# Optimization experiments

Measured on AMD Instinct MI355X. Metric: run time of the kernel, lower is better.

The kernel has to match this reference:

```python
import jax, jax.numpy as jnp
import numpy as np

N = 768          # nodes
E_HALF = 12288   # undirected edges (both directions added -> E = 24576)
P = 4096         # query pairs
H = 32           # hidden_dim_1wl == hidden_dim_2wl
MAX_X = 100
EPS = 1e-5
LAYER1 = 2


def setup_inputs() -> dict:
    key = jax.random.key(0)
    ks = jax.random.split(key, 12)
    s = 0.1
    x = jax.random.randint(ks[0], (N,), 0, MAX_X + 1)
    half = jax.random.randint(ks[1], (2, E_HALF), 0, N)
    ei = jnp.concatenate([half, half[::-1]], axis=1)          # symmetric edge set [2,E]
    pos = jax.random.randint(ks[2], (P, 2), 0, N)
    emb = jax.random.normal(ks[3], (MAX_X + 1, H)) * s
    gcn_W = jax.random.normal(ks[4], (LAYER1, H, H)) * s
    gcn_b = jnp.zeros((LAYER1, H))
    mlp1_W = jax.random.normal(ks[5], (2 * H, H)) * s
    mlp1_b = jnp.zeros((H,))
    mlp2_W = jax.random.normal(ks[6], (2 * H, H)) * s
    mlp2_b = jnp.zeros((H,))
    mlp3_W = jax.random.normal(ks[7], (H + 1, H)) * s
    mlp3_b = jnp.zeros((H,))
    lin_W = jax.random.normal(ks[8], (2 * H, 1)) * s
    lin_b = jnp.zeros((1,))
    return dict(x=x, ei=ei, pos=pos, emb=emb, gcn_W=gcn_W, gcn_b=gcn_b,
                mlp1_W=mlp1_W, mlp1_b=mlp1_b, mlp2_W=mlp2_W, mlp2_b=mlp2_b,
                mlp3_W=mlp3_W, mlp3_b=mlp3_b, lin_W=lin_W, lin_b=lin_b)


def _graph_norm(h):
    # PyG-style GraphNorm with default params (mean_scale=1, weight=1, bias=0)
    h = h - h.mean(0)
    return h * jax.lax.rsqrt((h * h).mean(0) + EPS)


def reference(x, ei, pos, emb, gcn_W, gcn_b, mlp1_W, mlp1_b,
              mlp2_W, mlp2_b, mlp3_W, mlp3_b, lin_W, lin_b):
    n = x.shape[0]
    d = emb.shape[1]
    h = emb[x]                                                 # [n,H] (dropout=0)
    # --- GCNConv stack: Ahat = D^-1/2 (A+I) D^-1/2 ---
    A = jnp.zeros((n, n), h.dtype).at[ei[0], ei[1]].set(1.0)
    Ahat = A + jnp.eye(n, dtype=h.dtype)
    dinv = jax.lax.rsqrt(Ahat.sum(1))
    An = Ahat * dinv[:, None] * dinv[None, :]
    for l in range(gcn_W.shape[0]):
        h = An @ (h @ gcn_W[l]) + gcn_b[l]
        h = jax.nn.relu(_graph_norm(h))                        # GraphNorm + ReLU
    # --- pair features ---
    xx = h[pos[:, 0]] * h[pos[:, 1]]                           # [P,H]
    val = jnp.concatenate([h[ei[0]], h[ei[1]]], 1)             # [E,2H]
    xe = jax.nn.relu(val @ mlp1_W + mlp1_b)                    # mlps_1
    mul = jax.nn.relu(val @ mlp2_W + mlp2_b)                   # mlps_2[0]
    # --- sparse_bmm as dense [n,n,d] contraction (coalesce sums duplicates -> .add) ---
    Xd = jnp.zeros((n, n, d), h.dtype).at[ei[0], ei[1]].add(xe)
    Md = jnp.zeros((n, n, d), h.dtype).at[ei[0], ei[1]].add(mul)
    C = jnp.einsum('ikd,kjd->ijd', Xd, Md)                     # x_{ij} = sum_k x_{ik}*mul_{kj}
    # support of the sparse result: 2-hop pairs union original edges (sparse_cat)
    adj_b = jnp.zeros((n, n), bool).at[ei[0], ei[1]].set(True)
    af = adj_b.astype(h.dtype)
    mask = ((af @ af) > 0) | adj_b
    ind = af[..., None]                                        # ones-column for original edges
    value = jnp.concatenate([C, ind], -1)                      # [n,n,H+1]
    z = value @ mlp3_W + mlp3_b                                # mlps_3[0]
    # GraphNorm over the edge support only (faithful to sparse values())
    m = mask.astype(h.dtype)[..., None]
    cnt = m.sum()
    mean = (z * m).sum((0, 1)) / cnt
    z = z - mean
    var = ((z * z) * m).sum((0, 1)) / cnt
    z = jax.nn.relu(z * jax.lax.rsqrt(var + EPS))
    # x * sm: multiply by transposed values; zero outside support (= add_zero)
    sym = z * jnp.swapaxes(z, 0, 1) * m
    pair = sym[pos[:, 0], pos[:, 1]]                           # [P,H] (edge_list gather)
    out = jnp.concatenate([pair, xx], 1) @ lin_W + lin_b       # lin_dir -> [P,1]
    return out
```

## Files before the change

kernel.cpp:

```cpp
#include <hip/hip_runtime.h>
#include <hip/hip_bf16.h>

#define NN 768
#define NE 24576
#define NPOS 4096
#define NCELL (NN*NN)
#define NBLK 2304
#define NBIG 2304
#define BCELLS 256
#define CAP 4
#define NREP 16

typedef __hip_bfloat16 bf16;

__device__ __forceinline__ float ldf(const void* p, int i, int mode) {
    return mode ? __bfloat162float(((const bf16*)p)[i]) : ((const float*)p)[i];
}
__device__ __forceinline__ float aread(float* p) { return atomicAdd(p, 0.f); }
__device__ __forceinline__ int areadi(int* p) { return atomicAdd(p, 0); }

template<int D, int HALF>
__device__ __forceinline__ void redRound(float* v, int lane) {
#pragma unroll
    for (int i = 0; i < HALF; i++) {
        float snd = (lane & D) ? v[i] : v[i + HALF];
        float r = __shfl_xor(snd, D);
        v[i] = ((lane & D) ? v[i + HALF] : v[i]) + r;
    }
}

#define DOT4(Z, A, W) Z += A.x * W.x + A.y * W.y + A.z * W.z + A.w * W.w

#define BLO(u) __uint_as_float((u) << 16)
#define BHI(u) __uint_as_float((u) & 0xFFFF0000u)

#define GATHB(rec, q0,q1,q2,q3,q4,q5,q6,q7) { \
    const uint4* xr = xep4b + (int)((unsigned)(rec).x & 0x7FFFu) * 4; \
    const uint4* mr = mulp4b + (int)((unsigned)(rec).y & 0x7FFFu) * 4; \
    uint4 xA = xr[0], xB = xr[1], xC = xr[2], xD = xr[3]; \
    uint4 mA = mr[0], mB = mr[1], mC = mr[2], mD = mr[3]; \
    q0.x += BLO(xA.x)*BLO(mA.x); q0.y += BHI(xA.x)*BHI(mA.x); \
    q0.z += BLO(xA.y)*BLO(mA.y); q0.w += BHI(xA.y)*BHI(mA.y); \
    q1.x += BLO(xA.z)*BLO(mA.z); q1.y += BHI(xA.z)*BHI(mA.z); \
    q1.z += BLO(xA.w)*BLO(mA.w); q1.w += BHI(xA.w)*BHI(mA.w); \
    q2.x += BLO(xB.x)*BLO(mB.x); q2.y += BHI(xB.x)*BHI(mB.x); \
    q2.z += BLO(xB.y)*BLO(mB.y); q2.w += BHI(xB.y)*BHI(mB.y); \
    q3.x += BLO(xB.z)*BLO(mB.z); q3.y += BHI(xB.z)*BHI(mB.z); \
    q3.z += BLO(xB.w)*BLO(mB.w); q3.w += BHI(xB.w)*BHI(mB.w); \
    q4.x += BLO(xC.x)*BLO(mC.x); q4.y += BHI(xC.x)*BHI(mC.x); \
    q4.z += BLO(xC.y)*BLO(mC.y); q4.w += BHI(xC.y)*BHI(mC.y); \
    q5.x += BLO(xC.z)*BLO(mC.z); q5.y += BHI(xC.z)*BHI(mC.z); \
    q5.z += BLO(xC.w)*BLO(mC.w); q5.w += BHI(xC.w)*BHI(mC.w); \
    q6.x += BLO(xD.x)*BLO(mD.x); q6.y += BHI(xD.x)*BHI(mD.x); \
    q6.z += BLO(xD.y)*BLO(mD.y); q6.w += BHI(xD.y)*BHI(mD.y); \
    q7.x += BLO(xD.z)*BLO(mD.z); q7.y += BHI(xD.z)*BHI(mD.z); \
    q7.z += BLO(xD.w)*BLO(mD.w); q7.w += BHI(xD.w)*BHI(mD.w); }

__global__ void k_scatter(const int* __restrict__ ei, int* __restrict__ cell, int* __restrict__ rowlen,
                          int* __restrict__ row_ptr, float* __restrict__ dinv, int* __restrict__ dc,
                          const void* __restrict__ gW, const void* __restrict__ gB,
                          const void* __restrict__ m1W, const void* __restrict__ m1B,
                          const void* __restrict__ m2W, const void* __restrict__ m2B,
                          const void* __restrict__ m3W, const void* __restrict__ m3B,
                          const void* __restrict__ lW,  const void* __restrict__ lB,
                          const void* __restrict__ emb, int* __restrict__ modeg,
                          float* __restrict__ gwf, float* __restrict__ gbf,
                          float* __restrict__ w1f, float* __restrict__ b1f,
                          float* __restrict__ w2f, float* __restrict__ b2f,
                          float* __restrict__ w3q, float* __restrict__ linf, float* __restrict__ linb) {
    int t = threadIdx.x;
    if (blockIdx.x == 96) {
        __shared__ int bad;
        if (t == 0) bad = 0;
        __syncthreads();
        int local = 0;
        for (int i = t; i < 3232; i += 256) {
            float a = fabsf(__bfloat162float(((const bf16*)emb)[i]));
            if (!(a < 100.f)) local = 1;
        }
        if (local) atomicOr(&bad, 1);
        __syncthreads();
        int mode = bad ? 0 : 1;
        if (t == 0) *modeg = mode;
        for (int i = t; i < 2048; i += 256) {
            gwf[i] = ldf(gW, i, mode);
            w1f[i] = ldf(m1W, i, mode);
            w2f[i] = ldf(m2W, i, mode);
        }
        for (int i = t; i < 64; i += 256) { gbf[i] = ldf(gB, i, mode); linf[i] = ldf(lW, i, mode); }
        if (t < 32) { b1f[t] = ldf(m1B, t, mode); b2f[t] = ldf(m2B, t, mode); }
        for (int i = t; i < 1056; i += 256) { int c = i >> 5, d = i & 31; w3q[d * 36 + c] = ldf(m3W, i, mode); }
        if (t < 32) { w3q[t * 36 + 33] = ldf(m3B, t, mode); w3q[t * 36 + 34] = 0.f; w3q[t * 36 + 35] = 0.f; }
        if (t == 0) linb[0] = ldf(lB, 0, mode);
        return;
    }
    __shared__ int amlast;
    __shared__ int sI[256];
    int e = blockIdx.x * 256 + t;
    int a = ei[e], b = ei[NE + e];
    if ((unsigned)a < (unsigned)NN && (unsigned)b < (unsigned)NN) {
        int old = atomicAdd(&cell[a * NN + b], 1);
        if (old == 0) atomicAdd(&rowlen[a], 1);
    }
    __syncthreads();
    if (t == 0) { __threadfence(); amlast = (atomicAdd(dc, 1) == 95) ? 1 : 0; }
    __syncthreads();
    if (!amlast) return;
    int i0 = 3 * t;
    int r0 = areadi(&rowlen[i0]), r1 = areadi(&rowlen[i0 + 1]), r2 = areadi(&rowlen[i0 + 2]);
    dinv[i0]     = rsqrtf((float)r0 + 1.f);
    dinv[i0 + 1] = rsqrtf((float)r1 + 1.f);
    dinv[i0 + 2] = rsqrtf((float)r2 + 1.f);
    int s3 = r0 + r1 + r2;
    sI[t] = s3;
    __syncthreads();
    for (int off = 1; off < 256; off <<= 1) {
        int tmp = (t >= off) ? sI[t - off] : 0;
        __syncthreads();
        sI[t] += tmp;
        __syncthreads();
    }
    int excl = sI[t] - s3;
    row_ptr[i0] = excl;
    row_ptr[i0 + 1] = excl + r0;
    row_ptr[i0 + 2] = excl + r0 + r1;
    if (t == 255) row_ptr[NN] = sI[255];
}

__global__ void k_fill(int* __restrict__ cell, const int* __restrict__ row_ptr, int* __restrict__ cursor,
                       int* __restrict__ col_idx, float* __restrict__ cntv, int* __restrict__ pr_row,
                       const int* __restrict__ rowlen, int* __restrict__ rtot,
                       const int* __restrict__ x, const void* __restrict__ emb,
                       const int* __restrict__ modep, float* __restrict__ bufA) {
    int t = threadIdx.x;
    int b = blockIdx.x;
    if (b < NBLK) {
        int idx = b * 256 + t;
        int i = idx / NN;
        int j = idx - i * NN;
        int cv = cell[idx];
        if (cv > 0) {
            int p = row_ptr[i] + atomicAdd(&cursor[i], 1);
            col_idx[p] = j; cntv[p] = (float)cv; pr_row[p] = i;
            cell[idx] = p;
            atomicAdd(&rtot[i], rowlen[j]);
        } else cell[idx] = -1;
    } else {
        int idx = (b - NBLK) * 256 + t;
        int i = idx >> 5, k = idx & 31;
        int xi = x[i]; if (xi < 0) xi = 0; if (xi > 100) xi = 100;
        bufA[idx] = ldf(emb, xi * 32 + k, *modep);
    }
}

__global__ void k_aggmw0(const int* __restrict__ rtot, int* __restrict__ row_base,
                         const int* __restrict__ row_ptr, const int* __restrict__ col_idx,
                         const float* __restrict__ bufA, const float* __restrict__ dinv,
                         const float* __restrict__ gwf, const float* __restrict__ gbf,
                         float* __restrict__ bufB) {
    int t = threadIdx.x;
    if (blockIdx.x == 0) {
        __shared__ int sI[256];
        int r3[3]; int s3 = 0;
#pragma unroll
        for (int q = 0; q < 3; q++) { r3[q] = rtot[3 * t + q]; s3 += r3[q]; }
        sI[t] = s3;
        __syncthreads();
        for (int off = 1; off < 256; off <<= 1) {
            int tmp = (t >= off) ? sI[t - off] : 0;
            __syncthreads();
            sI[t] += tmp;
            __syncthreads();
        }
        int run = sI[t] - s3;
        row_base[3 * t] = run;
        row_base[3 * t + 1] = run + r3[0];
        row_base[3 * t + 2] = run + r3[0] + r3[1];
        return;
    }
    __shared__ float sg8[8][32];
    __shared__ float agg[32];
    int sgi = t >> 5, k = t & 31;
    int i = blockIdx.x - 1;
    int base = row_ptr[i], len = row_ptr[i + 1] - base;
    float di = dinv[i];
    float acc = (sgi == 0) ? di * bufA[i * 32 + k] : 0.f;
    for (int e = sgi; e < len; e += 8) {
        int c = col_idx[base + e];
        acc += dinv[c] * bufA[c * 32 + k];
    }
    sg8[sgi][k] = acc;
    __syncthreads();
    if (t < 32) {
        float s = 0.f;
#pragma unroll
        for (int q = 0; q < 8; q++) s += sg8[q][k];
        agg[k] = di * s;
    }
    __syncthreads();
    if (t < 32) {
        int d = k;
        float s = gbf[d];
#pragma unroll
        for (int kk = 0; kk < 32; kk++) s += agg[kk] * gwf[kk * 32 + d];
        bufB[i * 32 + d] = s;
    }
}

__global__ void k_hist(const int* __restrict__ row_ptr, const int* __restrict__ col_idx,
                       const int* __restrict__ row_base,
                       int* __restrict__ pcur, int2* __restrict__ paths2, int cap,
                       const float* __restrict__ bufB, const float* __restrict__ dinv,
                       const float* __restrict__ gwf, const float* __restrict__ gbf,
                       float* __restrict__ bufA, float* __restrict__ stats1) {
    __shared__ float r1[256], r2[256];
    __shared__ float nmean[32], nrstd[32];
    __shared__ int hist[NN];
    __shared__ int sc[256];
    __shared__ float sg8[8][32];
    __shared__ float agg[32];
    int t = threadIdx.x;
    int i = blockIdx.x;

    {
        int dd = t & 31, g = t >> 5;
        float s = 0.f, s2 = 0.f;
        for (int r = g; r < NN; r += 8) { float v = bufB[r * 32 + dd]; s += v; s2 += v * v; }
        r1[t] = s; r2[t] = s2;
        __syncthreads();
        if (t < 32) {
            float a = 0.f, b2 = 0.f;
            for (int k = 0; k < 8; k++) { a += r1[k * 32 + t]; b2 += r2[k * 32 + t]; }
            float mean = a / (float)NN;
            float var = b2 / (float)NN - mean * mean;
            nmean[t] = mean;
            nrstd[t] = rsqrtf(fmaxf(var, 0.f) + 1e-5f);
        }
    }

    int base = row_ptr[i], len = row_ptr[i + 1] - base;
    int rb = row_base[i];
    int wave = t >> 6, lane = t & 63;
    int sub = lane >> 5, l2 = lane & 31;
    for (int j = t; j < NN; j += 256) hist[j] = 0;
    __syncthreads();

    for (int ee = wave * 2 + sub; ee < len; ee += 8) {
        int k = col_idx[base + ee];
        int kb = row_ptr[k], ke = row_ptr[k + 1];
        for (int e = kb + l2; e < ke; e += 32) atomicAdd(&hist[col_idx[e]], 1);
    }
    __syncthreads();
    int h0 = hist[3 * t], h1 = hist[3 * t + 1], h2 = hist[3 * t + 2];
    int s3 = h0 + h1 + h2;
    sc[t] = s3;
    __syncthreads();
    for (int off = 1; off < 256; off <<= 1) {
        int tmp = (t >= off) ? sc[t - off] : 0;
        __syncthreads();
        sc[t] += tmp;
        __syncthreads();
    }
    int excl = sc[t] - s3;
    int n0 = i * NN + 3 * t;
    pcur[n0]     = rb + excl + h0;
    pcur[n0 + 1] = rb + excl + h0 + h1;
    pcur[n0 + 2] = rb + excl + h0 + h1 + h2;
    hist[3 * t] = excl;
    hist[3 * t + 1] = excl + h0;
    hist[3 * t + 2] = excl + h0 + h1;
    __syncthreads();

    for (int ee = wave * 2 + sub; ee < len; ee += 8) {
        int e1 = base + ee;
        int k = col_idx[e1];
        int kb = row_ptr[k], ke = row_ptr[k + 1];
        for (int e = kb + l2; e < ke; e += 32) {
            int j = col_idx[e];
            int slot = rb + atomicAdd(&hist[j], 1);
            if (slot < cap) {
                unsigned n2 = (unsigned)(i * NN + j);
                paths2[slot] = make_int2((int)((unsigned)e1 | ((n2 & 0x1FFFFu) << 15)),
                                         (int)((unsigned)e  | ((n2 >> 17) << 15)));
            }
        }
    }
    __syncthreads();

    {
        int sgi = t >> 5, k = t & 31;
        float mk = nmean[k], rk = nrstd[k];
        float di = dinv[i];
        float acc = (sgi == 0) ? di * fmaxf((bufB[i * 32 + k] - mk) * rk, 0.f) : 0.f;
        for (int e = sgi; e < len; e += 8) {
            int c = col_idx[base + e];
            acc += dinv[c] * fmaxf((bufB[c * 32 + k] - mk) * rk, 0.f);
        }
        sg8[sgi][k] = acc;
        __syncthreads();
        if (t < 32) {
            float s = 0.f;
#pragma unroll
            for (int q = 0; q < 8; q++) s += sg8[q][k];
            agg[k] = di * s;
        }
        __syncthreads();
        if (t < 32) {
            int d = k;
            const float* W = gwf + 1024;
            float s = gbf[32 + d];
#pragma unroll
            for (int kk = 0; kk < 32; kk++) s += agg[kk] * W[kk * 32 + d];
            bufA[i * 32 + d] = s;
            float* rep = stats1 + (blockIdx.x & (NREP - 1)) * 80;
            atomicAdd(&rep[d], s);
            atomicAdd(&rep[32 + d], s * s);
        }
    }
}

__global__ void k_emlp(const float* __restrict__ bufA, const float* __restrict__ stats1,
                       const int* __restrict__ row_ptr, const int* __restrict__ col_idx,
                       const int* __restrict__ pr_row, const float* __restrict__ cntv,
                       const float* __restrict__ w1f, const float* __restrict__ b1f,
                       const float* __restrict__ w2f, const float* __restrict__ b2f,
                       bf16* __restrict__ xepb, bf16* __restrict__ mulpb, float* __restrict__ h) {
    __shared__ float nmean[32], nrstd[32];
    int t = threadIdx.x;
    int b = blockIdx.x;
    if (t < 32) {
        float s = 0.f, s2 = 0.f;
#pragma unroll
        for (int r = 0; r < NREP; r++) { s += stats1[r * 80 + t]; s2 += stats1[r * 80 + 32 + t]; }
        float mean = s / (float)NN;
        float var = s2 / (float)NN - mean * mean;
        nmean[t] = mean;
        nrstd[t] = rsqrtf(fmaxf(var, 0.f) + 1e-5f);
    }
    __syncthreads();
    if (b < 3072) {
        int d = t & 31;
        int p = b * 8 + (t >> 5);
        if (p >= row_ptr[NN]) {
            if (p < NE) { xepb[p * 32 + d] = __float2bfloat16(0.f); mulpb[p * 32 + d] = __float2bfloat16(0.f); }
            return;
        }
        int i = pr_row[p], j = col_idx[p];
        float a1 = b1f[d], a2 = b2f[d];
#pragma unroll
        for (int c = 0; c < 32; c++) {
            float hv = fmaxf((bufA[i * 32 + c] - nmean[c]) * nrstd[c], 0.f);
            a1 += hv * w1f[c * 32 + d];
            a2 += hv * w2f[c * 32 + d];
        }
#pragma unroll
        for (int c = 0; c < 32; c++) {
            float hv = fmaxf((bufA[j * 32 + c] - nmean[c]) * nrstd[c], 0.f);
            a1 += hv * w1f[(32 + c) * 32 + d];
            a2 += hv * w2f[(32 + c) * 32 + d];
        }
        float cv = cntv[p];
        xepb[p * 32 + d]  = __float2bfloat16(cv * fmaxf(a1, 0.f));
        mulpb[p * 32 + d] = __float2bfloat16(cv * fmaxf(a2, 0.f));
    } else {
        int idx = (b - 3072) * 256 + t;
        int d = idx & 31;
        h[idx] = fmaxf((bufA[idx] - nmean[d]) * nrstd[d], 0.f);
    }
}

__global__ __launch_bounds__(256, 4) void k_big(const int* __restrict__ pcur,
                                                const int2* __restrict__ paths2,
                                                const int* __restrict__ cellA,
                                                const bf16* __restrict__ xepb, const bf16* __restrict__ mulpb,
                                                const float* __restrict__ w3q,
                                                float* __restrict__ stats, int* __restrict__ done,
                                                float* __restrict__ nrm, int cap) {
    __shared__ float qbuf[64 * 32];
    __shared__ int qps[64], qpe[64];
    __shared__ float sS1[32], sS2[32];
    __shared__ float sCm;
    __shared__ int amlast;
    __shared__ int qcnt;
    const uint4* xep4b = (const uint4*)xepb;
    const uint4* mulp4b = (const uint4*)mulpb;
    int t = threadIdx.x;
    int b = blockIdx.x;
    int cell0 = b * BCELLS;
    int wid = t >> 6, lane = t & 63, half = lane >> 5, d = lane & 31;

    if (t == 0) { sCm = 0.f; qcnt = 0; }
    if (t < 32) { sS1[t] = 0.f; sS2[t] = 0.f; }
    int myn = cell0 + t;
    int mp1 = pcur[myn];
    int mp0 = (myn == 0) ? 0 : pcur[myn - 1];
    int madj = cellA[myn];
    if (mp0 > cap) mp0 = cap;
    if (mp1 > cap) mp1 = cap;
    __syncthreads();

    int len = mp1 - mp0;
    int take = (len > CAP) ? CAP : len;
    int myq = -1;
    if (len > CAP) {
        int s = atomicAdd(&qcnt, 1);
        if (s < 64) { myq = s; qps[s] = mp0 + CAP; qpe[s] = mp1; }
    }
    int pm = cap - 1; if (pm < 0) pm = 0;
    int i0 = mp0, i1 = mp0 + 1, i2 = mp0 + 2, i3 = mp0 + 3;
    if (i0 > pm) i0 = pm; if (i1 > pm) i1 = pm; if (i2 > pm) i2 = pm; if (i3 > pm) i3 = pm;
    int2 r0 = paths2[i0];
    int2 r1 = paths2[i1];
    int2 r2 = paths2[i2];
    int2 r3 = paths2[i3];
    float4 q0 = {0.f,0.f,0.f,0.f}, q1 = q0, q2 = q0, q3 = q0, q4 = q0, q5 = q0, q6 = q0, q7 = q0;
    if (take > 0) GATHB(r0, q0, q1, q2, q3, q4, q5, q6, q7);
    if (take > 1) GATHB(r1, q0, q1, q2, q3, q4, q5, q6, q7);
    if (take > 2) GATHB(r2, q0, q1, q2, q3, q4, q5, q6, q7);
    if (take > 3) GATHB(r3, q0, q1, q2, q3, q4, q5, q6, q7);
    __syncthreads();

    int nq = qcnt; if (nq > 64) nq = 64;
    for (int e = wid; e < nq; e += 4) {
        int pe = qpe[e];
        float acc = 0.f;
        for (int q = qps[e] + half; q < pe; q += 2) {
            int2 r = paths2[q];
            acc += __bfloat162float(xepb[(int)((unsigned)r.x & 0x7FFFu) * 32 + d]) *
                   __bfloat162float(mulpb[(int)((unsigned)r.y & 0x7FFFu) * 32 + d]);
        }
        acc += __shfl_xor(acc, 32);
        if (lane < 32) qbuf[e * 32 + lane] = acc;
    }
    __syncthreads();
    if (myq >= 0) {
        const float4* qb = (const float4*)(qbuf + myq * 32);
        float4 a0 = qb[0], a1 = qb[1], a2 = qb[2], a3 = qb[3];
        float4 a4 = qb[4], a5 = qb[5], a6 = qb[6], a7 = qb[7];
        q0.x += a0.x; q0.y += a0.y; q0.z += a0.z; q0.w += a0.w;
        q1.x += a1.x; q1.y += a1.y; q1.z += a1.z; q1.w += a1.w;
        q2.x += a2.x; q2.y += a2.y; q2.z += a2.z; q2.w += a2.w;
        q3.x += a3.x; q3.y += a3.y; q3.z += a3.z; q3.w += a3.w;
        q4.x += a4.x; q4.y += a4.y; q4.z += a4.z; q4.w += a4.w;
        q5.x += a5.x; q5.y += a5.y; q5.z += a5.z; q5.w += a5.w;
        q6.x += a6.x; q6.y += a6.y; q6.z += a6.z; q6.w += a6.w;
        q7.x += a7.x; q7.y += a7.y; q7.z += a7.z; q7.w += a7.w;
    }

    float af = (madj >= 0) ? 1.f : 0.f;
    float msk = (len > 0 || madj >= 0) ? 1.f : 0.f;
#pragma unroll
    for (int ch = 0; ch < 2; ch++) {
        float v[32];
#pragma unroll
        for (int j = 0; j < 16; j++) {
            int dd = ch * 16 + j;
            const float4* wr = (const float4*)(w3q + dd * 36);
            float4 wv = wr[8];
            float za = wv.y + af * wv.x;
            wv = wr[0]; DOT4(za, q0, wv);
            wv = wr[1]; DOT4(za, q1, wv);
            wv = wr[2]; DOT4(za, q2, wv);
            wv = wr[3]; DOT4(za, q3, wv);
            wv = wr[4]; DOT4(za, q4, wv);
            wv = wr[5]; DOT4(za, q5, wv);
            wv = wr[6]; DOT4(za, q6, wv);
            wv = wr[7]; DOT4(za, q7, wv);
            v[j] = msk * za;
            v[16 + j] = msk * za * za;
        }
#pragma unroll
        for (int i2r = 0; i2r < 32; i2r++) v[i2r] += __shfl_xor(v[i2r], 32);
        redRound<16, 16>(v, lane);
        redRound<8, 8>(v, lane);
        redRound<4, 4>(v, lane);
        redRound<2, 2>(v, lane);
        redRound<1, 1>(v, lane);
        if (lane < 32) {
            if (lane < 16) atomicAdd(&sS1[ch * 16 + lane], v[0]);
            else           atomicAdd(&sS2[ch * 16 + lane - 16], v[0]);
        }
    }
    {
        float cm2 = msk;
        for (int off = 32; off >= 1; off >>= 1) cm2 += __shfl_xor(cm2, off);
        if (lane == 0) atomicAdd(&sCm, cm2);
    }
    __syncthreads();
    float* srep = stats + (b & (NREP - 1)) * 80;
    if (t < 32) {
        atomicAdd(&srep[t], sS1[t]);
        atomicAdd(&srep[32 + t], sS2[t]);
    }
    if (t == 32) atomicAdd(&srep[64], sCm);
    __syncthreads();
    if (t == 0) {
        __threadfence();
        amlast = (atomicAdd(done, 1) == NBIG - 1) ? 1 : 0;
    }
    __syncthreads();
    if (amlast && t < 32) {
        float sum1 = 0.f, sum2 = 0.f;
        for (int r = 0; r < NREP; r++) {
            sum1 += aread(&stats[r * 80 + t]);
            sum2 += aread(&stats[r * 80 + 32 + t]);
        }
        float cmt = 0.f;
        for (int r = 0; r < NREP; r++) cmt += aread(&stats[r * 80 + 64]);
        if (cmt < 1.f) cmt = 1.f;
        float mean = sum1 / cmt;
        float var = sum2 / cmt - mean * mean;
        nrm[t] = mean;
        nrm[32 + t] = rsqrtf(fmaxf(var, 0.f) + 1e-5f);
    }
}

__global__ void k_out(const int* __restrict__ pos, const int* __restrict__ pcur,
                      const int2* __restrict__ paths2,
                      const int* __restrict__ cell,
                      const bf16* __restrict__ xepb, const bf16* __restrict__ mulpb,
                      const float* __restrict__ h,
                      const float* __restrict__ w3q,
                      const float* __restrict__ nrm,
                      const float* __restrict__ linf, const float* __restrict__ linb,
                      const int* __restrict__ modep, int cap, void* __restrict__ outp) {
    __shared__ float Cb[4][2][32];
    int t = threadIdx.x;
    int w = t >> 6, lane = t & 63, d = lane & 31, dir = lane >> 5;
    int p = blockIdx.x * 4 + w;
    int a = pos[2 * p], b = pos[2 * p + 1];
    if ((unsigned)a >= (unsigned)NN) a = 0;
    if ((unsigned)b >= (unsigned)NN) b = 0;
    int r = dir ? b : a;
    int cc = dir ? a : b;
    int n = r * NN + cc;
    int p1 = pcur[n];
    int p0 = (n == 0) ? 0 : pcur[n - 1];
    if (p0 > cap) p0 = cap; if (p1 > cap) p1 = cap;
    float acc = 0.f;
    for (int q = p0; q < p1; q++) {
        int2 rec = paths2[q];
        int e1 = (int)((unsigned)rec.x & 0x7FFFu);
        int e2 = (int)((unsigned)rec.y & 0x7FFFu);
        acc += __bfloat162float(xepb[e1 * 32 + d]) * __bfloat162float(mulpb[e2 * 32 + d]);
    }
    Cb[w][dir][d] = acc;
    bool adj = cell[n] >= 0;
    float msk = (p1 > p0 || adj) ? 1.f : 0.f;
    __syncthreads();
    float z = w3q[d * 36 + 33] + (adj ? 1.f : 0.f) * w3q[d * 36 + 32];
#pragma unroll
    for (int c = 0; c < 32; c++) z += Cb[w][dir][c] * w3q[d * 36 + c];
    float zn = fmaxf((z - nrm[d]) * nrm[32 + d], 0.f);
    float zp = __shfl_xor(zn, 32);
    float symd = msk * zn * zp;
    float xxd = h[a * 32 + d] * h[b * 32 + d];
    float contrib = symd * linf[d] + xxd * linf[32 + d];
    for (int off = 16; off >= 1; off >>= 1) contrib += __shfl_xor(contrib, off);
    if (lane == 0) {
        float v = contrib + linb[0];
        v = fminf(fmaxf(v, -1e4f), 1e4f);
        if (*modep) ((bf16*)outp)[p] = __float2bfloat16(v);
        else        ((float*)outp)[p] = v;
    }
}

extern "C" void kernel_launch(void* const* d_in, const int* in_sizes, int n_in,
                              void* d_out, int out_size, void* d_ws, size_t ws_size,
                              hipStream_t stream) {
    const void* px  = d_in[0];  const void* pei = d_in[1];  const void* ppos = d_in[2];
    const void* pemb = d_in[3]; const void* pgW = d_in[4];  const void* pgB  = d_in[5];
    const void* pm1W = d_in[6]; const void* pm1B = d_in[7]; const void* pm2W = d_in[8];
    const void* pm2B = d_in[9]; const void* pm3W = d_in[10]; const void* pm3B = d_in[11];
    const void* plW = d_in[12]; const void* plB = d_in[13];
    {
        int c2048 = 0, c64 = 0, c32 = 0;
        for (int i = 0; i < n_in; i++) {
            int s = in_sizes[i]; const void* p = d_in[i];
            switch (s) {
                case 768:   px = p; break;
                case 49152: pei = p; break;
                case 8192:  ppos = p; break;
                case 3232:  pemb = p; break;
                case 2048:  if (c2048 == 0) pgW = p; else if (c2048 == 1) pm1W = p; else pm2W = p; c2048++; break;
                case 64:    if (c64 == 0) pgB = p; else plW = p; c64++; break;
                case 32:    if (c32 == 0) pm1B = p; else if (c32 == 1) pm2B = p; else pm3B = p; c32++; break;
                case 1056:  pm3W = p; break;
                case 1:     plB = p; break;
                default: break;
            }
        }
    }

    char* ws = (char*)d_ws;
    size_t off = 0;
    auto alloc = [&](size_t bytes) -> void* {
        void* pp = ws + off;
        off += (bytes + 255) & ~(size_t)255;
        return pp;
    };
    int*   cell    = (int*)alloc(NCELL * 4);
    int*   rowlen  = (int*)alloc(NN * 4);
    int*   rtot    = (int*)alloc(NN * 4);
    int*   cursor  = (int*)alloc(NN * 4);
    float* stats   = (float*)alloc(NREP * 80 * 4);
    float* stats1  = (float*)alloc(NREP * 80 * 4);
    int*   dcs     = (int*)alloc(8 * 4);
    size_t zerolen = (ws + off) - (char*)cell;
    int*   pcur    = (int*)alloc(NCELL * 4);
    int*   row_base= (int*)alloc(NN * 4);
    int*   row_ptr = (int*)alloc((NN + 1) * 4);
    int*   col_idx = (int*)alloc(NE * 4);
    float* cntv    = (float*)alloc(NE * 4);
    int*   pr_row  = (int*)alloc(NE * 4);
    float* dinv    = (float*)alloc(NN * 4);
    float* h       = (float*)alloc(NN * 32 * 4);
    float* bufA    = (float*)alloc(NN * 32 * 4);
    float* bufB    = (float*)alloc(NN * 32 * 4);
    bf16*  xep     = (bf16*)alloc(NE * 32 * 2);
    bf16*  mulp    = (bf16*)alloc(NE * 32 * 2);
    float* nrm     = (float*)alloc(64 * 4);
    float* gwf     = (float*)alloc(2048 * 4);
    float* gbf     = (float*)alloc(64 * 4);
    float* w1f     = (float*)alloc(2048 * 4);
    float* b1f     = (float*)alloc(32 * 4);
    float* w2f     = (float*)alloc(2048 * 4);
    float* b2f     = (float*)alloc(32 * 4);
    float* w3q     = (float*)alloc(32 * 36 * 4);
    float* linf    = (float*)alloc(64 * 4);
    float* linb    = (float*)alloc(4);
    int*   modeg   = (int*)alloc(4);
    size_t remain = (ws_size > off) ? (ws_size - off) : 0;
    int cap = (int)(remain / 8);
    if (cap > (1 << 20)) cap = (1 << 20);
    int2*  paths2  = (int2*)alloc((size_t)cap * 8);

    hipMemsetAsync(cell, 0, zerolen, stream);
    k_scatter<<<97, 256, 0, stream>>>((const int*)pei, cell, rowlen, row_ptr, dinv, &dcs[0],
                                      pgW, pgB, pm1W, pm1B, pm2W, pm2B, pm3W, pm3B, plW, plB,
                                      pemb, modeg, gwf, gbf, w1f, b1f, w2f, b2f, w3q, linf, linb);
    k_fill<<<NBLK + 96, 256, 0, stream>>>(cell, row_ptr, cursor, col_idx, cntv, pr_row,
                                          rowlen, rtot, (const int*)px, pemb, modeg, bufA);
    k_aggmw0<<<1 + NN, 256, 0, stream>>>(rtot, row_base, row_ptr, col_idx, bufA, dinv, gwf, gbf, bufB);
    k_hist<<<NN, 256, 0, stream>>>(row_ptr, col_idx, row_base, pcur, paths2, cap, bufB,
                                   dinv, gwf, gbf, bufA, stats1);
    k_emlp<<<3072 + 96, 256, 0, stream>>>(bufA, stats1, row_ptr, col_idx, pr_row, cntv,
                                          w1f, b1f, w2f, b2f, xep, mulp, h);
    k_big<<<NBIG, 256, 0, stream>>>(pcur, paths2, cell, xep, mulp,
                                    w3q, stats, &dcs[1], nrm, cap);
    k_out<<<NPOS / 4, 256, 0, stream>>>((const int*)ppos, pcur, paths2, cell, xep, mulp, h,
                                        w3q, nrm, linf, linb, modeg, cap, d_out);
}
```

Baseline: 283.2 us.

## Split each cell across two threads to halve register accumulators in k_big

Each cell of the n×n pair grid is now handled by two threads, each owning 16 of the 32 hidden channels. Blocks cover 128 cells instead of 256, so the grid doubles, and launch bounds are raised to target 8 blocks per SM. The goal is to cut per-thread register pressure (half the float4 accumulators and gather loads) so occupancy rises and gather latency is better hidden. The cost is an extra shuffle per output channel to combine the partial mlp3 dot products, twice as many blocks contending on the stats atomics, and more duplicated per-cell index loads.

Result: slower. 496.8 us (+75.4%).

```diff
diff --git a/kernel.cpp b/kernel.cpp
--- a/kernel.cpp
+++ b/kernel.cpp
@@ -6,8 +6,8 @@
 #define NPOS 4096
 #define NCELL (NN*NN)
 #define NBLK 2304
-#define NBIG 2304
-#define BCELLS 256
+#define NBIG 4608
+#define BCELLS 128
 #define CAP 4
 #define NREP 16
 
@@ -34,11 +34,7 @@
 #define BLO(u) __uint_as_float((u) << 16)
 #define BHI(u) __uint_as_float((u) & 0xFFFF0000u)
 
-#define GATHB(rec, q0,q1,q2,q3,q4,q5,q6,q7) { \
-    const uint4* xr = xep4b + (int)((unsigned)(rec).x & 0x7FFFu) * 4; \
-    const uint4* mr = mulp4b + (int)((unsigned)(rec).y & 0x7FFFu) * 4; \
-    uint4 xA = xr[0], xB = xr[1], xC = xr[2], xD = xr[3]; \
-    uint4 mA = mr[0], mB = mr[1], mC = mr[2], mD = mr[3]; \
+#define ACCUM16(xA,xB, mA,mB, q0,q1,q2,q3) { \
     q0.x += BLO(xA.x)*BLO(mA.x); q0.y += BHI(xA.x)*BHI(mA.x); \
     q0.z += BLO(xA.y)*BLO(mA.y); q0.w += BHI(xA.y)*BHI(mA.y); \
     q1.x += BLO(xA.z)*BLO(mA.z); q1.y += BHI(xA.z)*BHI(mA.z); \
@@ -46,15 +42,7 @@
     q2.x += BLO(xB.x)*BLO(mB.x); q2.y += BHI(xB.x)*BHI(mB.x); \
     q2.z += BLO(xB.y)*BLO(mB.y); q2.w += BHI(xB.y)*BHI(mB.y); \
     q3.x += BLO(xB.z)*BLO(mB.z); q3.y += BHI(xB.z)*BHI(mB.z); \
-    q3.z += BLO(xB.w)*BLO(mB.w); q3.w += BHI(xB.w)*BHI(mB.w); \
-    q4.x += BLO(xC.x)*BLO(mC.x); q4.y += BHI(xC.x)*BHI(mC.x); \
-    q4.z += BLO(xC.y)*BLO(mC.y); q4.w += BHI(xC.y)*BHI(mC.y); \
-    q5.x += BLO(xC.z)*BLO(mC.z); q5.y += BHI(xC.z)*BHI(mC.z); \
-    q5.z += BLO(xC.w)*BLO(mC.w); q5.w += BHI(xC.w)*BHI(mC.w); \
-    q6.x += BLO(xD.x)*BLO(mD.x); q6.y += BHI(xD.x)*BHI(mD.x); \
-    q6.z += BLO(xD.y)*BLO(mD.y); q6.w += BHI(xD.y)*BHI(mD.y); \
-    q7.x += BLO(xD.z)*BLO(mD.z); q7.y += BHI(xD.z)*BHI(mD.z); \
-    q7.z += BLO(xD.w)*BLO(mD.w); q7.w += BHI(xD.w)*BHI(mD.w); }
+    q3.z += BLO(xB.w)*BLO(mB.w); q3.w += BHI(xB.w)*BHI(mB.w); }
 
 __global__ void k_scatter(const int* __restrict__ ei, int* __restrict__ cell, int* __restrict__ rowlen,
                           int* __restrict__ row_ptr, float* __restrict__ dinv, int* __restrict__ dc,
@@ -369,7 +357,7 @@
     }
 }
 
-__global__ __launch_bounds__(256, 4) void k_big(const int* __restrict__ pcur,
+__global__ __launch_bounds__(256, 8) void k_big(const int* __restrict__ pcur,
                                                 const int2* __restrict__ paths2,
                                                 const int* __restrict__ cellA,
                                                 const bf16* __restrict__ xepb, const bf16* __restrict__ mulpb,
@@ -378,6 +366,7 @@
                                                 float* __restrict__ nrm, int cap) {
     __shared__ float qbuf[64 * 32];
     __shared__ int qps[64], qpe[64];
+    __shared__ int qsl[BCELLS];
     __shared__ float sS1[32], sS2[32];
     __shared__ float sCm;
     __shared__ int amlast;
@@ -387,11 +376,14 @@
     int t = threadIdx.x;
     int b = blockIdx.x;
     int cell0 = b * BCELLS;
-    int wid = t >> 6, lane = t & 63, half = lane >> 5, d = lane & 31;
+    int lane = t & 63;
+    int cl = t >> 1;
+    int ph = t & 1;
 
     if (t == 0) { sCm = 0.f; qcnt = 0; }
     if (t < 32) { sS1[t] = 0.f; sS2[t] = 0.f; }
-    int myn = cell0 + t;
+    if (t < BCELLS) qsl[t] = -1;
+    int myn = cell0 + cl;
     int mp1 = pcur[myn];
     int mp0 = (myn == 0) ? 0 : pcur[myn - 1];
     int madj = cellA[myn];
@@ -401,10 +393,9 @@
 
     int len = mp1 - mp0;
     int take = (len > CAP) ? CAP : len;
-    int myq = -1;
-    if (len > CAP) {
+    if (len > CAP && ph == 0) {
         int s = atomicAdd(&qcnt, 1);
-        if (s < 64) { myq = s; qps[s] = mp0 + CAP; qpe[s] = mp1; }
+        if (s < 64) { qsl[cl] = s; qps[s] = mp0 + CAP; qpe[s] = mp1; }
     }
     int pm = cap - 1; if (pm < 0) pm = 0;
     int i0 = mp0, i1 = mp0 + 1, i2 = mp0 + 2, i3 = mp0 + 3;
@@ -413,42 +404,53 @@
     int2 r1 = paths2[i1];
     int2 r2 = paths2[i2];
     int2 r3 = paths2[i3];
-    float4 q0 = {0.f,0.f,0.f,0.f}, q1 = q0, q2 = q0, q3 = q0, q4 = q0, q5 = q0, q6 = q0, q7 = q0;
-    if (take > 0) GATHB(r0, q0, q1, q2, q3, q4, q5, q6, q7);
-    if (take > 1) GATHB(r1, q0, q1, q2, q3, q4, q5, q6, q7);
-    if (take > 2) GATHB(r2, q0, q1, q2, q3, q4, q5, q6, q7);
-    if (take > 3) GATHB(r3, q0, q1, q2, q3, q4, q5, q6, q7);
+    float4 q0 = {0.f,0.f,0.f,0.f}, q1 = q0, q2 = q0, q3 = q0;
+#pragma unroll
+    for (int pp = 0; pp < CAP; pp++) {
+        int2 rr = (pp == 0) ? r0 : (pp == 1) ? r1 : (pp == 2) ? r2 : r3;
+        if (take > pp) {
+            int e1 = rr.x & 0x7FFF;
+            int e2 = rr.y & 0x7FFF;
+            const uint4* mr = mulp4b + e2 * 4 + ph * 2;
+            uint4 mA = mr[0], mB = mr[1];
+            const uint4* xr = xep4b + e1 * 4 + ph * 2;
+            uint4 xA = xr[0], xB = xr[1];
+            ACCUM16(xA, xB, mA, mB, q0, q1, q2, q3);
+        }
+    }
     __syncthreads();
 
     int nq = qcnt; if (nq > 64) nq = 64;
-    for (int e = wid; e < nq; e += 4) {
-        int pe = qpe[e];
-        float acc = 0.f;
-        for (int q = qps[e] + half; q < pe; q += 2) {
-            int2 r = paths2[q];
-            acc += __bfloat162float(xepb[(int)((unsigned)r.x & 0x7FFFu) * 32 + d]) *
-                   __bfloat162float(mulpb[(int)((unsigned)r.y & 0x7FFFu) * 32 + d]);
-        }
-        acc += __shfl_xor(acc, 32);
-        if (lane < 32) qbuf[e * 32 + lane] = acc;
-    }
-    __syncthreads();
-    if (myq >= 0) {
-        const float4* qb = (const float4*)(qbuf + myq * 32);
-        float4 a0 = qb[0], a1 = qb[1], a2 = qb[2], a3 = qb[3];
-        float4 a4 = qb[4], a5 = qb[5], a6 = qb[6], a7 = qb[7];
-        q0.x += a0.x; q0.y += a0.y; q0.z += a0.z; q0.w += a0.w;
-        q1.x += a1.x; q1.y += a1.y; q1.z += a1.z; q1.w += a1.w;
-        q2.x += a2.x; q2.y += a2.y; q2.z += a2.z; q2.w += a2.w;
-        q3.x += a3.x; q3.y += a3.y; q3.z += a3.z; q3.w += a3.w;
-        q4.x += a4.x; q4.y += a4.y; q4.z += a4.z; q4.w += a4.w;
-        q5.x += a5.x; q5.y += a5.y; q5.z += a5.z; q5.w += a5.w;
-        q6.x += a6.x; q6.y += a6.y; q6.z += a6.z; q6.w += a6.w;
-        q7.x += a7.x; q7.y += a7.y; q7.z += a7.z; q7.w += a7.w;
+    {
+        int wid = t >> 6, h32 = lane >> 5, d = lane & 31;
+        for (int e = wid; e < nq; e += 4) {
+            int pe = qpe[e];
+            float acc = 0.f;
+            for (int q = qps[e] + h32; q < pe; q += 2) {
+                int2 r = paths2[q];
+                acc += __bfloat162float(xepb[(int)((unsigned)r.x & 0x7FFFu) * 32 + d]) *
+                       __bfloat162float(mulpb[(int)((unsigned)r.y & 0x7FFFu) * 32 + d]);
+            }
+            acc += __shfl_xor(acc, 32);
+            if (lane < 32) qbuf[e * 32 + lane] = acc;
+        }
+    }
+    __syncthreads();
+    {
+        int myq = qsl[cl];
+        if (myq >= 0) {
+            const float4* qb = (const float4*)(qbuf + myq * 32 + ph * 16);
+            float4 a0 = qb[0], a1 = qb[1], a2 = qb[2], a3 = qb[3];
+            q0.x += a0.x; q0.y += a0.y; q0.z += a0.z; q0.w += a0.w;
+            q1.x += a1.x; q1.y += a1.y; q1.z += a1.z; q1.w += a1.w;
+            q2.x += a2.x; q2.y += a2.y; q2.z += a2.z; q2.w += a2.w;
+            q3.x += a3.x; q3.y += a3.y; q3.z += a3.z; q3.w += a3.w;
+        }
     }
 
     float af = (madj >= 0) ? 1.f : 0.f;
     float msk = (len > 0 || madj >= 0) ? 1.f : 0.f;
+    float mske = ph ? 0.f : msk;
 #pragma unroll
     for (int ch = 0; ch < 2; ch++) {
         float v[32];
@@ -457,17 +459,16 @@
             int dd = ch * 16 + j;
             const float4* wr = (const float4*)(w3q + dd * 36);
             float4 wv = wr[8];
-            float za = wv.y + af * wv.x;
-            wv = wr[0]; DOT4(za, q0, wv);
-            wv = wr[1]; DOT4(za, q1, wv);
-            wv = wr[2]; DOT4(za, q2, wv);
-            wv = wr[3]; DOT4(za, q3, wv);
-            wv = wr[4]; DOT4(za, q4, wv);
-            wv = wr[5]; DOT4(za, q5, wv);
-            wv = wr[6]; DOT4(za, q6, wv);
-            wv = wr[7]; DOT4(za, q7, wv);
-            v[j] = msk * za;
-            v[16 + j] = msk * za * za;
+            float za = ph ? 0.f : (wv.y + af * wv.x);
+            float4 w0 = wr[ph * 4 + 0], w1 = wr[ph * 4 + 1];
+            float4 w2 = wr[ph * 4 + 2], w3v = wr[ph * 4 + 3];
+            DOT4(za, q0, w0);
+            DOT4(za, q1, w1);
+            DOT4(za, q2, w2);
+            DOT4(za, q3, w3v);
+            za += __shfl_xor(za, 1);
+            v[j] = mske * za;
+            v[16 + j] = mske * za * za;
         }
 #pragma unroll
         for (int i2r = 0; i2r < 32; i2r++) v[i2r] += __shfl_xor(v[i2r], 32);
@@ -482,7 +483,7 @@
         }
     }
     {
-        float cm2 = msk;
+        float cm2 = mske;
         for (int off = 32; off >= 1; off >>= 1) cm2 += __shfl_xor(cm2, off);
         if (lane == 0) atomicAdd(&sCm, cm2);
     }
```
